# Kernel optimization log

Hardware: AMD Instinct MI355X
Metric: run time of the kernel (lower is better)

## Reference

```python
import jax, jax.numpy as jnp
import numpy as np

B, T, E, D = 8, 2048, 1024, 64  # batch, seq_len, n_emb, head_dim

def setup_inputs() -> dict:
    key = jax.random.key(0)
    ks = jax.random.split(key, 4)
    scale = 1.0 / np.sqrt(E)
    return {
        "x": jax.random.normal(ks[0], (B, T, E), dtype=jnp.float32),
        "Wq": jax.random.normal(ks[1], (E, D), dtype=jnp.float32) * scale,
        "bq": jnp.zeros((D,), dtype=jnp.float32),
        "Wk": jax.random.normal(ks[2], (E, D), dtype=jnp.float32) * scale,
        "bk": jnp.zeros((D,), dtype=jnp.float32),
        "Wv": jax.random.normal(ks[3], (E, D), dtype=jnp.float32) * scale,
        "bv": jnp.zeros((D,), dtype=jnp.float32),
    }

def reference(x, Wq, bq, Wk, bk, Wv, bv):
    # QKV projections: [B,T,E] @ [E,D] -> [B,T,D]
    q = x @ Wq + bq
    k = x @ Wk + bk
    v = x @ Wv + bv
    d = q.shape[-1]
    # scaled dot-product scores [B,T,T]
    wei = jnp.einsum('btd,bsd->bts', q, k) * (d ** -0.5)
    # causal mask: position t attends to s <= t
    t = wei.shape[1]
    causal = jnp.tril(jnp.ones((t, t), dtype=bool))
    wei = jnp.where(causal, wei, -jnp.inf)
    wei = jax.nn.softmax(wei, axis=-1)
    # attention output [B,T,D]
    return jnp.einsum('bts,bsd->btd', wei, v)
```

## Files before the change

kernel.cpp:

```cpp
#include <hip/hip_runtime.h>
#include <math.h>


#define B_   8
#define T_   2048
#define E_   1024
#define D_   64
#define BT_  (B_ * T_)

typedef __attribute__((ext_vector_type(8))) short s16x8;
typedef __attribute__((ext_vector_type(4))) short s16x4;
typedef __attribute__((ext_vector_type(4))) float f32x4;

__device__ __forceinline__ short f2bf(float f) {
    union { float f; unsigned u; } a; a.f = f;
    unsigned r = a.u + 0x7fffu + ((a.u >> 16) & 1u);
    return (short)(r >> 16);
}

#define MFMA16(a, b, c) __builtin_amdgcn_mfma_f32_16x16x32_bf16((a), (b), (c), 0, 0, 0)

#define DPPF(x, ctrl) __builtin_bit_cast(float, \
    __builtin_amdgcn_update_dpp(0, __builtin_bit_cast(int, (x)), (ctrl), 0xF, 0xF, true))

__device__ __forceinline__ float rsum16(float x) {
    x += DPPF(x, 0xB1);
    x += DPPF(x, 0x4E);
    x += DPPF(x, 0x124);
    x += DPPF(x, 0x128);
    return x;
}

__global__ __launch_bounds__(256) void wtrans_kernel(
    const float* __restrict__ Wq, const float* __restrict__ Wk,
    const float* __restrict__ Wv, short* __restrict__ Wt)
{
    __shared__ float sT[64][65];
    const int sel = blockIdx.x >> 4;
    const int k0  = (blockIdx.x & 15) * 64;
    const float* W = sel == 0 ? Wq : (sel == 1 ? Wk : Wv);
    const int t  = threadIdx.x;
    const int kr = t >> 4, c4 = (t & 15) * 4;
    #pragma unroll
    for (int i = 0; i < 4; ++i) {
        float4 v = *(const float4*)&W[(size_t)(k0 + kr + i * 16) * D_ + c4];
        sT[kr + i * 16][c4 + 0] = v.x; sT[kr + i * 16][c4 + 1] = v.y;
        sT[kr + i * 16][c4 + 2] = v.z; sT[kr + i * 16][c4 + 3] = v.w;
    }
    __syncthreads();
    #pragma unroll
    for (int i = 0; i < 4; ++i) {
        int n  = (t >> 4) + i * 16;
        int kk = (t & 15) * 4;
        s16x4 o;
        o.x = f2bf(sT[kk + 0][n]); o.y = f2bf(sT[kk + 1][n]);
        o.z = f2bf(sT[kk + 2][n]); o.w = f2bf(sT[kk + 3][n]);
        *(s16x4*)&Wt[(size_t)(sel * 64 + n) * E_ + k0 + kk] = o;
    }
}

__global__ __launch_bounds__(256) void qkv_kernel(
    const float* __restrict__ x, const short* __restrict__ Wt,
    const float* __restrict__ bq, const float* __restrict__ bk,
    const float* __restrict__ bv,
    short* __restrict__ Qg, short* __restrict__ Kg, short* __restrict__ VTg)
{
    __shared__ short sX[2][32 * 76];
    const int tid  = threadIdx.x;
    const int lane = tid & 63;
    const int w    = tid >> 6;
    const int l15  = lane & 15, quad = lane >> 4;
    const int t0   = blockIdx.x * 32;
    const int bb   = t0 >> 11;

    const int srow = tid >> 3;
    const int skc  = (tid & 7) * 8;
    const float* px = &x[(size_t)(t0 + srow) * E_ + skc];

    f32x4 acc[3][2];
    #pragma unroll
    for (int a = 0; a < 3; ++a)
        #pragma unroll
        for (int h = 0; h < 2; ++h)
            acc[a][h] = (f32x4){0.f, 0.f, 0.f, 0.f};

    float4 lda0 = *(const float4*)px;
    float4 lda1 = *(const float4*)(px + 4);
    float4 ldb0 = *(const float4*)(px + 64);
    float4 ldb1 = *(const float4*)(px + 68);

    int buf = 0;
    for (int k0 = 0; k0 < E_; k0 += 64) {
        s16x8 pk;
        pk[0] = f2bf(lda0.x); pk[1] = f2bf(lda0.y);
        pk[2] = f2bf(lda0.z); pk[3] = f2bf(lda0.w);
        pk[4] = f2bf(lda1.x); pk[5] = f2bf(lda1.y);
        pk[6] = f2bf(lda1.z); pk[7] = f2bf(lda1.w);
        *(s16x8*)&sX[buf][srow * 76 + skc] = pk;
        __syncthreads();

        lda0 = ldb0; lda1 = ldb1;
        if (k0 + 128 < E_) {
            const float* p2 = px + k0 + 128;
            ldb0 = *(const float4*)p2;
            ldb1 = *(const float4*)(p2 + 4);
        }

        s16x8 aw[3][2];
        #pragma unroll
        for (int t3 = 0; t3 < 3; ++t3) {
            const short* pw = &Wt[(size_t)((w * 3 + t3) * 16 + l15) * E_ + k0 + quad * 8];
            aw[t3][0] = *(const s16x8*)pw;
            aw[t3][1] = *(const s16x8*)(pw + 32);
        }
        s16x8 bxf[2][2];
        #pragma unroll
        for (int h = 0; h < 2; ++h) {
            bxf[h][0] = *(const s16x8*)&sX[buf][(h * 16 + l15) * 76 + quad * 8];
            bxf[h][1] = *(const s16x8*)&sX[buf][(h * 16 + l15) * 76 + 32 + quad * 8];
        }
        #pragma unroll
        for (int t3 = 0; t3 < 3; ++t3)
            #pragma unroll
            for (int h = 0; h < 2; ++h) {
                acc[t3][h] = MFMA16(aw[t3][0], bxf[h][0], acc[t3][h]);
                acc[t3][h] = MFMA16(aw[t3][1], bxf[h][1], acc[t3][h]);
            }
        buf ^= 1;
    }

    __syncthreads();
    short* sVT = &sX[0][0];

    #pragma unroll
    for (int t3 = 0; t3 < 3; ++t3) {
        const int nt = w * 3 + t3;
        const int fb = (nt & 3) * 16 + quad * 4;
        const float* bias = nt < 4 ? bq : (nt < 8 ? bk : bv);
        f32x4 bsv = *(const f32x4*)&bias[fb];
        #pragma unroll
        for (int h = 0; h < 2; ++h) {
            const int tok = t0 + h * 16 + l15;
            f32x4 v = acc[t3][h] + bsv;
            if (nt < 4) {
                v *= 0.125f;
                s16x4 o = { f2bf(v[0]), f2bf(v[1]), f2bf(v[2]), f2bf(v[3]) };
                *(s16x4*)&Qg[(size_t)tok * D_ + fb] = o;
            } else if (nt < 8) {
                s16x4 o = { f2bf(v[0]), f2bf(v[1]), f2bf(v[2]), f2bf(v[3]) };
                *(s16x4*)&Kg[(size_t)tok * D_ + fb] = o;
            } else {
                const int lt = h * 16 + l15;
                #pragma unroll
                for (int r = 0; r < 4; ++r)
                    sVT[(fb + r) * 48 + lt] = f2bf(v[r]);
            }
        }
    }
    __syncthreads();
    {
        const int d  = tid >> 2;
        const int tq = (tid & 3) * 8;
        s16x8 vv = *(const s16x8*)&sVT[d * 48 + tq];
        *(s16x8*)&VTg[(size_t)(bb * D_ + d) * T_ + (t0 & (T_ - 1)) + tq] = vv;
    }
}

__global__ __launch_bounds__(256, 2) void attn_kernel(
    const short* __restrict__ Qg, const short* __restrict__ Kg,
    const short* __restrict__ VTg, float* __restrict__ out)
{
    __shared__ char smem[20736];
    short* sP = (short*)smem;
    float* sO = (float*)smem;
    float* sl = (float*)(smem + 20480);

    const int tid  = threadIdx.x;
    const int lane = tid & 63;
    const int w    = tid >> 6;
    const int l15  = lane & 15, quad = lane >> 4;
    const int b    = blockIdx.x & 7;
    const int pr   = blockIdx.x >> 3;
    const int jA   = pr, jB = 127 - pr;
    const int tqA  = jA * 16, tqB = jB * 16;
    const int nchA = (jA >> 2) + 1, nchB = (jB >> 2) + 1;
    const int tot  = nchA + nchB;
    const int seg  = (tot + 3) >> 2;
    const int c0   = w * seg;
    const int c1   = (c0 + seg < tot) ? c0 + seg : tot;

    const size_t qoffA = ((size_t)b * T_ + tqA + l15) * D_ + quad * 8;
    const s16x8 aqA0 = *(const s16x8*)&Qg[qoffA];
    const s16x8 aqA1 = *(const s16x8*)&Qg[qoffA + 32];
    const size_t qoffB = ((size_t)b * T_ + tqB + l15) * D_ + quad * 8;
    const s16x8 aqB0 = *(const s16x8*)&Qg[qoffB];
    const s16x8 aqB1 = *(const s16x8*)&Qg[qoffB + 32];

    f32x4 oA[4], oB[4];
    float lA[4] = {0.f, 0.f, 0.f, 0.f}, lB[4] = {0.f, 0.f, 0.f, 0.f};
    #pragma unroll
    for (int nt = 0; nt < 4; ++nt) {
        oA[nt] = (f32x4){0.f, 0.f, 0.f, 0.f};
        oB[nt] = (f32x4){0.f, 0.f, 0.f, 0.f};
    }

    const short* kb = Kg  + (size_t)b * T_ * D_;
    const short* vb = VTg + (size_t)b * D_ * T_;
    short* sPw = sP + w * (16 * 72);

    auto s0_of = [&](int c) {
        return (c < nchA) ? c * 64 : (c - nchA) * 64;
    };

    s16x8 kc[4][2];
    {
        const int s0 = s0_of(c0);
        #pragma unroll
        for (int nt = 0; nt < 4; ++nt) {
            const short* pk = kb + (size_t)(s0 + nt * 16 + l15) * D_ + quad * 8;
            kc[nt][0] = *(const s16x8*)pk;
            kc[nt][1] = *(const s16x8*)(pk + 32);
        }
    }

    for (int c = c0; c < c1; ++c) {
        const bool isA = (c < nchA);
        const int cc   = isA ? c : c - nchA;
        const int tq   = isA ? tqA : tqB;
        const int nch  = isA ? nchA : nchB;
        const int s0   = cc * 64;

        s16x8 nk[4][2];
        {
            const int sn = s0_of(c + 1 < c1 ? c + 1 : c);
            #pragma unroll
            for (int nt = 0; nt < 4; ++nt) {
                const short* pk = kb + (size_t)(sn + nt * 16 + l15) * D_ + quad * 8;
                nk[nt][0] = *(const s16x8*)pk;
                nk[nt][1] = *(const s16x8*)(pk + 32);
            }
        }

        const s16x8 q0 = isA ? aqA0 : aqB0;
        const s16x8 q1 = isA ? aqA1 : aqB1;
        const f32x4 zz = (f32x4){0.f, 0.f, 0.f, 0.f};
        f32x4 sacc[4];
        #pragma unroll
        for (int nt = 0; nt < 4; ++nt) {
            sacc[nt] = MFMA16(q0, kc[nt][0], zz);
            sacc[nt] = MFMA16(q1, kc[nt][1], sacc[nt]);
        }

        s16x8 bv[4][2];
        #pragma unroll
        for (int nt = 0; nt < 4; ++nt) {
            const short* pv = vb + (size_t)(nt * 16 + l15) * T_ + s0 + quad * 8;
            bv[nt][0] = *(const s16x8*)pv;
            bv[nt][1] = *(const s16x8*)(pv + 32);
        }

        const bool diag = (cc == nch - 1);
        float p[4][4];
        #pragma unroll
        for (int nt = 0; nt < 4; ++nt)
            #pragma unroll
            for (int r = 0; r < 4; ++r) {
                float e = __expf(sacc[nt][r]);
                if (diag && (s0 + nt * 16 + l15 > tq + quad * 4 + r)) e = 0.f;
                p[nt][r] = e;
            }

        #pragma unroll
        for (int nt = 0; nt < 4; ++nt)
            #pragma unroll
            for (int r = 0; r < 4; ++r)
                sPw[(quad * 4 + r) * 72 + nt * 16 + l15] = f2bf(p[nt][r]);
        s16x8 ap0 = *(const s16x8*)&sPw[l15 * 72 + quad * 8];
        s16x8 ap1 = *(const s16x8*)&sPw[l15 * 72 + 32 + quad * 8];

        if (isA) {
            #pragma unroll
            for (int r = 0; r < 4; ++r)
                lA[r] += (p[0][r] + p[1][r]) + (p[2][r] + p[3][r]);
            #pragma unroll
            for (int nt = 0; nt < 4; ++nt) {
                oA[nt] = MFMA16(ap0, bv[nt][0], oA[nt]);
                oA[nt] = MFMA16(ap1, bv[nt][1], oA[nt]);
            }
        } else {
            #pragma unroll
            for (int r = 0; r < 4; ++r)
                lB[r] += (p[0][r] + p[1][r]) + (p[2][r] + p[3][r]);
            #pragma unroll
            for (int nt = 0; nt < 4; ++nt) {
                oB[nt] = MFMA16(ap0, bv[nt][0], oB[nt]);
                oB[nt] = MFMA16(ap1, bv[nt][1], oB[nt]);
            }
        }

        #pragma unroll
        for (int nt = 0; nt < 4; ++nt) {
            kc[nt][0] = nk[nt][0]; kc[nt][1] = nk[nt][1];
        }
    }

    f32x4 lvA, lvB;
    #pragma unroll
    for (int r = 0; r < 4; ++r) { lvA[r] = rsum16(lA[r]); lvB[r] = rsum16(lB[r]); }

    const int d  = tid & 63;
    const int rb = (tid >> 6) * 4;

    __syncthreads();
    {
        float* sOw = sO + w * (64 * 20);
        #pragma unroll
        for (int nt = 0; nt < 4; ++nt)
            *(f32x4*)&sOw[(nt * 16 + l15) * 20 + quad * 4] = oA[nt];
        if (l15 == 0) *(f32x4*)&sl[w * 16 + quad * 4] = lvA;
    }
    __syncthreads();
    {
        f32x4 osum = (f32x4){0.f, 0.f, 0.f, 0.f};
        f32x4 lsum = (f32x4){0.f, 0.f, 0.f, 0.f};
        #pragma unroll
        for (int w2 = 0; w2 < 4; ++w2) {
            osum += *(const f32x4*)&sO[w2 * (64 * 20) + d * 20 + rb];
            lsum += *(const f32x4*)&sl[w2 * 16 + rb];
        }
        #pragma unroll
        for (int i = 0; i < 4; ++i)
            out[((size_t)b * T_ + tqA + rb + i) * D_ + d] = osum[i] / lsum[i];
    }

    __syncthreads();
    {
        float* sOw = sO + w * (64 * 20);
        #pragma unroll
        for (int nt = 0; nt < 4; ++nt)
            *(f32x4*)&sOw[(nt * 16 + l15) * 20 + quad * 4] = oB[nt];
        if (l15 == 0) *(f32x4*)&sl[w * 16 + quad * 4] = lvB;
    }
    __syncthreads();
    {
        f32x4 osum = (f32x4){0.f, 0.f, 0.f, 0.f};
        f32x4 lsum = (f32x4){0.f, 0.f, 0.f, 0.f};
        #pragma unroll
        for (int w2 = 0; w2 < 4; ++w2) {
            osum += *(const f32x4*)&sO[w2 * (64 * 20) + d * 20 + rb];
            lsum += *(const f32x4*)&sl[w2 * 16 + rb];
        }
        #pragma unroll
        for (int i = 0; i < 4; ++i)
            out[((size_t)b * T_ + tqB + rb + i) * D_ + d] = osum[i] / lsum[i];
    }
}

extern "C" void kernel_launch(void* const* d_in, const int* in_sizes, int n_in,
                              void* d_out, int out_size, void* d_ws, size_t ws_size,
                              hipStream_t stream) {
    (void)in_sizes; (void)n_in; (void)out_size; (void)ws_size;
    const float* x  = (const float*)d_in[0];
    const float* Wq = (const float*)d_in[1];
    const float* bq = (const float*)d_in[2];
    const float* Wk = (const float*)d_in[3];
    const float* bk = (const float*)d_in[4];
    const float* Wv = (const float*)d_in[5];
    const float* bv = (const float*)d_in[6];

    char* ws = (char*)d_ws;
    short* Qg  = (short*)(ws);
    short* Kg  = (short*)(ws + (size_t)2 * 1024 * 1024);
    short* VTg = (short*)(ws + (size_t)4 * 1024 * 1024);
    short* Wt  = (short*)(ws + (size_t)6 * 1024 * 1024);

    wtrans_kernel<<<48, 256, 0, stream>>>(Wq, Wk, Wv, Wt);
    qkv_kernel<<<BT_ / 32, 256, 0, stream>>>(x, Wt, bq, bk, bv, Qg, Kg, VTg);
    attn_kernel<<<B_ * 64, 256, 0, stream>>>(Qg, Kg, VTg, (float*)d_out);
}
```

Baseline: 161.7 us.

## Shrink QKV tile to 16 tokens and load x directly into MFMA registers

The QKV projection kernel now handles 16 tokens per block instead of 32, doubling the grid. Each lane loads its x fragment straight from global memory and converts it to bf16 in registers, which removes the shared-memory staging buffer and the per-iteration block barrier. As a result, each of the four waves converts the same x rows redundantly. Weight tiles are now reused across only 16 tokens, so weight traffic per token doubles. The V transpose now uses a small per-wave shared buffer without a block-wide sync.

```diff
diff --git a/kernel.cpp b/kernel.cpp
--- a/kernel.cpp
+++ b/kernel.cpp
@@ -65,104 +65,85 @@
     const float* __restrict__ bv,
     short* __restrict__ Qg, short* __restrict__ Kg, short* __restrict__ VTg)
 {
-    __shared__ short sX[2][32 * 76];
+    __shared__ short sVT[4][16 * 18];
     const int tid  = threadIdx.x;
     const int lane = tid & 63;
     const int w    = tid >> 6;
     const int l15  = lane & 15, quad = lane >> 4;
-    const int t0   = blockIdx.x * 32;
+    const int t0   = blockIdx.x * 16;
     const int bb   = t0 >> 11;
 
-    const int srow = tid >> 3;
-    const int skc  = (tid & 7) * 8;
-    const float* px = &x[(size_t)(t0 + srow) * E_ + skc];
-
-    f32x4 acc[3][2];
-    #pragma unroll
-    for (int a = 0; a < 3; ++a)
-        #pragma unroll
-        for (int h = 0; h < 2; ++h)
-            acc[a][h] = (f32x4){0.f, 0.f, 0.f, 0.f};
-
-    float4 lda0 = *(const float4*)px;
-    float4 lda1 = *(const float4*)(px + 4);
-    float4 ldb0 = *(const float4*)(px + 64);
-    float4 ldb1 = *(const float4*)(px + 68);
-
-    int buf = 0;
+    const float* px = &x[(size_t)(t0 + l15) * E_ + quad * 8];
+    const short* pwA[3];
+    #pragma unroll
+    for (int t3 = 0; t3 < 3; ++t3)
+        pwA[t3] = &Wt[(size_t)((w + 4 * t3) * 16 + l15) * E_ + quad * 8];
+
+    f32x4 acc[3];
+    #pragma unroll
+    for (int t3 = 0; t3 < 3; ++t3) acc[t3] = (f32x4){0.f, 0.f, 0.f, 0.f};
+
+    float4 xa[4], xb[4];
+    xa[0] = *(const float4*)(px + 0);  xa[1] = *(const float4*)(px + 4);
+    xa[2] = *(const float4*)(px + 32); xa[3] = *(const float4*)(px + 36);
+    xb[0] = *(const float4*)(px + 64); xb[1] = *(const float4*)(px + 68);
+    xb[2] = *(const float4*)(px + 96); xb[3] = *(const float4*)(px + 100);
+
     for (int k0 = 0; k0 < E_; k0 += 64) {
-        s16x8 pk;
-        pk[0] = f2bf(lda0.x); pk[1] = f2bf(lda0.y);
-        pk[2] = f2bf(lda0.z); pk[3] = f2bf(lda0.w);
-        pk[4] = f2bf(lda1.x); pk[5] = f2bf(lda1.y);
-        pk[6] = f2bf(lda1.z); pk[7] = f2bf(lda1.w);
-        *(s16x8*)&sX[buf][srow * 76 + skc] = pk;
-        __syncthreads();
-
-        lda0 = ldb0; lda1 = ldb1;
+        s16x8 b0, b1;
+        b0[0] = f2bf(xa[0].x); b0[1] = f2bf(xa[0].y);
+        b0[2] = f2bf(xa[0].z); b0[3] = f2bf(xa[0].w);
+        b0[4] = f2bf(xa[1].x); b0[5] = f2bf(xa[1].y);
+        b0[6] = f2bf(xa[1].z); b0[7] = f2bf(xa[1].w);
+        b1[0] = f2bf(xa[2].x); b1[1] = f2bf(xa[2].y);
+        b1[2] = f2bf(xa[2].z); b1[3] = f2bf(xa[2].w);
+        b1[4] = f2bf(xa[3].x); b1[5] = f2bf(xa[3].y);
+        b1[6] = f2bf(xa[3].z); b1[7] = f2bf(xa[3].w);
+
+        #pragma unroll
+        for (int i = 0; i < 4; ++i) xa[i] = xb[i];
         if (k0 + 128 < E_) {
             const float* p2 = px + k0 + 128;
-            ldb0 = *(const float4*)p2;
-            ldb1 = *(const float4*)(p2 + 4);
-        }
-
-        s16x8 aw[3][2];
+            xb[0] = *(const float4*)(p2 + 0);  xb[1] = *(const float4*)(p2 + 4);
+            xb[2] = *(const float4*)(p2 + 32); xb[3] = *(const float4*)(p2 + 36);
+        }
+
+        s16x8 a0[3], a1[3];
         #pragma unroll
         for (int t3 = 0; t3 < 3; ++t3) {
-            const short* pw = &Wt[(size_t)((w * 3 + t3) * 16 + l15) * E_ + k0 + quad * 8];
-            aw[t3][0] = *(const s16x8*)pw;
-            aw[t3][1] = *(const s16x8*)(pw + 32);
-        }
-        s16x8 bxf[2][2];
-        #pragma unroll
-        for (int h = 0; h < 2; ++h) {
-            bxf[h][0] = *(const s16x8*)&sX[buf][(h * 16 + l15) * 76 + quad * 8];
-            bxf[h][1] = *(const s16x8*)&sX[buf][(h * 16 + l15) * 76 + 32 + quad * 8];
-        }
-        #pragma unroll
-        for (int t3 = 0; t3 < 3; ++t3)
-            #pragma unroll
-            for (int h = 0; h < 2; ++h) {
-                acc[t3][h] = MFMA16(aw[t3][0], bxf[h][0], acc[t3][h]);
-                acc[t3][h] = MFMA16(aw[t3][1], bxf[h][1], acc[t3][h]);
-            }
-        buf ^= 1;
-    }
-
-    __syncthreads();
-    short* sVT = &sX[0][0];
-
-    #pragma unroll
-    for (int t3 = 0; t3 < 3; ++t3) {
-        const int nt = w * 3 + t3;
-        const int fb = (nt & 3) * 16 + quad * 4;
-        const float* bias = nt < 4 ? bq : (nt < 8 ? bk : bv);
-        f32x4 bsv = *(const f32x4*)&bias[fb];
-        #pragma unroll
-        for (int h = 0; h < 2; ++h) {
-            const int tok = t0 + h * 16 + l15;
-            f32x4 v = acc[t3][h] + bsv;
-            if (nt < 4) {
-                v *= 0.125f;
-                s16x4 o = { f2bf(v[0]), f2bf(v[1]), f2bf(v[2]), f2bf(v[3]) };
-                *(s16x4*)&Qg[(size_t)tok * D_ + fb] = o;
-            } else if (nt < 8) {
-                s16x4 o = { f2bf(v[0]), f2bf(v[1]), f2bf(v[2]), f2bf(v[3]) };
-                *(s16x4*)&Kg[(size_t)tok * D_ + fb] = o;
-            } else {
-                const int lt = h * 16 + l15;
-                #pragma unroll
-                for (int r = 0; r < 4; ++r)
-                    sVT[(fb + r) * 48 + lt] = f2bf(v[r]);
-            }
-        }
-    }
-    __syncthreads();
-    {
-        const int d  = tid >> 2;
-        const int tq = (tid & 3) * 8;
-        s16x8 vv = *(const s16x8*)&sVT[d * 48 + tq];
-        *(s16x8*)&VTg[(size_t)(bb * D_ + d) * T_ + (t0 & (T_ - 1)) + tq] = vv;
+            a0[t3] = *(const s16x8*)(pwA[t3] + k0);
+            a1[t3] = *(const s16x8*)(pwA[t3] + k0 + 32);
+        }
+        #pragma unroll
+        for (int t3 = 0; t3 < 3; ++t3) {
+            acc[t3] = MFMA16(a0[t3], b0, acc[t3]);
+            acc[t3] = MFMA16(a1[t3], b1, acc[t3]);
+        }
+    }
+
+    const int fb = w * 16 + quad * 4;
+    {
+        f32x4 v = acc[0] + *(const f32x4*)&bq[fb];
+        v *= 0.125f;
+        s16x4 o = { f2bf(v[0]), f2bf(v[1]), f2bf(v[2]), f2bf(v[3]) };
+        *(s16x4*)&Qg[(size_t)(t0 + l15) * D_ + fb] = o;
+    }
+    {
+        f32x4 v = acc[1] + *(const f32x4*)&bk[fb];
+        s16x4 o = { f2bf(v[0]), f2bf(v[1]), f2bf(v[2]), f2bf(v[3]) };
+        *(s16x4*)&Kg[(size_t)(t0 + l15) * D_ + fb] = o;
+    }
+    {
+        f32x4 v = acc[2] + *(const f32x4*)&bv[fb];
+        #pragma unroll
+        for (int r = 0; r < 4; ++r)
+            sVT[w][(quad * 4 + r) * 18 + l15] = f2bf(v[r]);
+        if (lane < 32) {
+            const int f = lane >> 1, half = lane & 1;
+            s16x8 vv = *(const s16x8*)&sVT[w][f * 18 + half * 8];
+            *(s16x8*)&VTg[(size_t)(bb * D_ + w * 16 + f) * T_
+                          + (t0 & (T_ - 1)) + half * 8] = vv;
+        }
     }
 }
 
@@ -375,6 +356,6 @@
     short* Wt  = (short*)(ws + (size_t)6 * 1024 * 1024);
 
     wtrans_kernel<<<48, 256, 0, stream>>>(Wq, Wk, Wv, Wt);
-    qkv_kernel<<<BT_ / 32, 256, 0, stream>>>(x, Wt, bq, bk, bv, Qg, Kg, VTg);
+    qkv_kernel<<<BT_ / 16, 256, 0, stream>>>(x, Wt, bq, bk, bv, Qg, Kg, VTg);
     attn_kernel<<<B_ * 64, 256, 0, stream>>>(Qg, Kg, VTg, (float*)d_out);
 }
```

Result: slower. 199.3 us (+23.3%).
